# Performance work log

Measured on AMD Instinct MI355X. Metric: run time of the kernel, lower is better.

Reference implementation:

```python
import jax, jax.numpy as jnp
import numpy as np

B, F_IN, F_OUT, D, K = 32, 64, 64, 512, 64


def setup_inputs() -> dict:
    key = jax.random.key(0)
    k1, k2, k3 = jax.random.split(key, 3)
    x = jax.random.normal(k1, (B, F_IN, D), dtype=jnp.float32)
    # Evaluated monomial-word operators: K matrices of size D x D
    word_ops = jax.random.normal(k2, (K, D, D), dtype=jnp.float32)
    # nn.init.uniform_ -> U[0,1)
    coeff = jax.random.uniform(k3, (F_OUT, F_IN, K), dtype=jnp.float32)
    return {"x": x, "word_ops": word_ops, "coeff": coeff}


def reference(x, word_ops, coeff):
    # Per sample in the torch code:
    #   evals[i, d, k] = (X @ W_k)[i, d] = sum_e X[i, e] * W[k, e, d]
    #   res = tensordot(coeff, evals, ([1, 2], [0, 2]))  -> [F_out, D]
    # Fully batched fused contraction (replaces the Python loop over batch):
    # evals: [B, F_in, D, K]
    evals = jnp.einsum('bie,ked->bidk', x, word_ops)
    # out: [B, F_out, D]
    out = jnp.einsum('oik,bidk->bod', coeff, evals)
    return out
```

## Files before the change

kernel.cpp:

```cpp
#include <hip/hip_runtime.h>
#include <hip/hip_bf16.h>


#define KK 32768

typedef __attribute__((ext_vector_type(8))) short bf16x8;
typedef __attribute__((ext_vector_type(4))) float f32x4;

__device__ __forceinline__ unsigned short f2bf(float f) {
  unsigned int u = __float_as_uint(f);
  return (unsigned short)((u + 0x7FFFu + ((u >> 16) & 1u)) >> 16);
}

__device__ __forceinline__ unsigned int pkbf2(float a, float b) {
  __hip_bfloat162 h = __float22bfloat162_rn(make_float2(a, b));
  return *(unsigned int*)&h;
}

__device__ __forceinline__ void gld16(void* lds, const void* g) {
  __builtin_amdgcn_global_load_lds((const __attribute__((address_space(1))) void*)g,
                                   (__attribute__((address_space(3))) void*)lds,
                                   16, 0, 0);
}

#define WAIT_VM0_LG0() asm volatile("s_waitcnt vmcnt(0) lgkmcnt(0)" ::: "memory")
#define WAIT_VM4()     asm volatile("s_waitcnt vmcnt(4)" ::: "memory")
#define WAIT_LG0()     asm volatile("s_waitcnt lgkmcnt(0)" ::: "memory")
#define BARRIER()      __builtin_amdgcn_s_barrier()
#define SCHEDB()       __builtin_amdgcn_sched_barrier(0)

__global__ __launch_bounds__(256) void prep_kern(const float* __restrict__ x,
                                                 const float* __restrict__ c,
                                                 const float* __restrict__ W,
                                                 unsigned short* __restrict__ xT,
                                                 unsigned short* __restrict__ cb,
                                                 unsigned short* __restrict__ WbT) {
  __shared__ float tile[64][133];
  int bx = blockIdx.x;
  int t = threadIdx.x;
  if (bx < 2048) {
    int k = bx >> 5, et = (bx >> 2) & 7, dq = bx & 3;
    const float* src = W + ((size_t)k * 512 + (size_t)et * 64) * 512 + dq * 128;
    int rr = t >> 5, c4 = t & 31;
#pragma unroll
    for (int p = 0; p < 8; p++) {
      int e = p * 8 + rr;
      float4 v = *(const float4*)(src + (size_t)e * 512 + c4 * 4);
      *(float4*)&tile[e][c4 * 4] = v;
    }
    __syncthreads();
    int ch = t & 7, dr = t >> 3;
#pragma unroll
    for (int p = 0; p < 4; p++) {
      int d = p * 32 + dr, e0 = ch * 8;
      uint4 o4;
      o4.x = pkbf2(tile[e0 + 0][d], tile[e0 + 1][d]);
      o4.y = pkbf2(tile[e0 + 2][d], tile[e0 + 3][d]);
      o4.z = pkbf2(tile[e0 + 4][d], tile[e0 + 5][d]);
      o4.w = pkbf2(tile[e0 + 6][d], tile[e0 + 7][d]);
      *(uint4*)(WbT + (size_t)(dq * 128 + d) * KK + k * 512 + et * 64 + e0) = o4;
    }
  } else if (bx < 2176) {
    int bx2 = bx - 2048;
    int b = bx2 >> 2, ec = bx2 & 3;
    const float* src = x + (size_t)b * 32768 + ec * 128;
    int rr = t >> 5, c4 = t & 31;
#pragma unroll
    for (int p = 0; p < 8; p++) {
      int i = p * 8 + rr;
      float4 v = *(const float4*)(src + (size_t)i * 512 + c4 * 4);
      *(float4*)&tile[i][c4 * 4] = v;
    }
    __syncthreads();
    unsigned short* dst = xT + (size_t)b * 32768 + ec * 128 * 64;
    int ch = t & 7, er = t >> 3;
#pragma unroll
    for (int p = 0; p < 4; p++) {
      int e = p * 32 + er, i0 = ch * 8;
      uint4 o4;
      o4.x = pkbf2(tile[i0 + 0][e], tile[i0 + 1][e]);
      o4.y = pkbf2(tile[i0 + 2][e], tile[i0 + 3][e]);
      o4.z = pkbf2(tile[i0 + 4][e], tile[i0 + 5][e]);
      o4.w = pkbf2(tile[i0 + 6][e], tile[i0 + 7][e]);
      *(uint4*)(dst + e * 64 + i0) = o4;
    }
  } else {
    int rb = bx - 2176;
    unsigned short* lds = (unsigned short*)tile;
    const float* src = c + (size_t)rb * 4096;
#pragma unroll
    for (int j = 0; j < 16; j++) {
      int idx = j * 256 + t;
      int r = idx >> 6, k = idx & 63;
      lds[r * 66 + k] = f2bf(src[idx]);
    }
    __syncthreads();
#pragma unroll
    for (int j = 0; j < 16; j++) {
      int idx = j * 256 + t;
      int k = idx >> 6, r = idx & 63;
      cb[(size_t)k * 4096 + rb * 64 + r] = lds[r * 66 + k];
    }
  }
}

__global__ __launch_bounds__(256, 2) void fused_kern(const unsigned short* __restrict__ xT,
                                                     const unsigned short* __restrict__ cb,
                                                     const unsigned short* __restrict__ Bt,
                                                     float* __restrict__ out) {
  __shared__ unsigned short u[128 * 64];
  __shared__ unsigned short Bs0[128 * 64];
  __shared__ unsigned short Bs1[128 * 64];
  __shared__ unsigned short ck[4 * 64 * 64];
  int bx = blockIdx.x;
  int ks = bx & 15, np = (bx >> 4) & 1, mt = bx >> 5;
  int m0 = mt * 128, n0 = np * 256, kw0 = ks * 4, b0 = mt * 2;
  int t = threadIdx.x;
  int wid = t >> 6, lane = t & 63, q = lane >> 4, l16 = lane & 15;
  int wmb = wid & 1;
  int wnh = wid >> 1;
  int srow = t >> 3;
  int cg = (t & 7) ^ (srow & 7);
  {
    const unsigned short* gc = cb + (size_t)kw0 * 4096;
#pragma unroll
    for (int j = 0; j < 8; j++) {
      int row = j * 32 + srow;
      gld16((char*)ck + (j * 256 + t) * 16, gc + (size_t)row * 64 + cg * 8);
    }
    const unsigned short* gb = Bt + (size_t)n0 * KK + (size_t)kw0 * 512;
#pragma unroll
    for (int j = 0; j < 4; j++)
      gld16((char*)Bs0 + (j * 256 + t) * 16, gb + (size_t)(j * 32 + srow) * KK + cg * 8);
  }
  f32x4 acc[4][8] = {};
  bf16x8 ax[4][2];
#pragma unroll 1
  for (int s = 0; s < 32; s++) {
    int k = s & 3, ec = s >> 2;
    f32x4 td[4][2];
    const unsigned short* ckk = ck + k * 4096;
    if (k != 0) {
      bf16x8 bc[2][2];
#pragma unroll
      for (int otl = 0; otl < 2; otl++)
#pragma unroll
        for (int k2 = 0; k2 < 2; k2++) {
          int o = (wnh * 2 + otl) * 16 + l16;
          int s2 = (k2 * 4 + q) ^ (o & 7);
          bc[otl][k2] = *(const bf16x8*)(ckk + o * 64 + s2 * 8);
        }
#pragma unroll
      for (int et = 0; et < 4; et++)
#pragma unroll
        for (int otl = 0; otl < 2; otl++) {
          td[et][otl] = (f32x4){0.f, 0.f, 0.f, 0.f};
#pragma unroll
          for (int k2 = 0; k2 < 2; k2++)
            td[et][otl] = __builtin_amdgcn_mfma_f32_16x16x32_bf16(ax[et][k2], bc[otl][k2],
                                                                  td[et][otl], 0, 0, 0);
        }
      WAIT_VM0_LG0(); BARRIER(); SCHEDB();
      {
        const unsigned short* gb = Bt + (size_t)(n0 + 128) * KK
                                      + (size_t)(kw0 + k) * 512 + ec * 64;
#pragma unroll
        for (int j = 0; j < 4; j++)
          gld16((char*)Bs1 + (j * 256 + t) * 16, gb + (size_t)(j * 32 + srow) * KK + cg * 8);
      }
    } else {
      WAIT_VM0_LG0(); BARRIER(); SCHEDB();
#pragma unroll
      for (int j = 0; j < 4; j++) {
        int row = j * 32 + srow;
        int bl = row >> 6, el = row & 63;
        gld16((char*)u + (j * 256 + t) * 16,
              xT + (size_t)(b0 + bl) * 32768 + (size_t)(ec * 64 + el) * 64 + cg * 8);
      }
      {
        const unsigned short* gb = Bt + (size_t)(n0 + 128) * KK
                                      + (size_t)kw0 * 512 + ec * 64;
#pragma unroll
        for (int j = 0; j < 4; j++)
          gld16((char*)Bs1 + (j * 256 + t) * 16, gb + (size_t)(j * 32 + srow) * KK + cg * 8);
      }
      WAIT_VM4(); BARRIER(); SCHEDB();
#pragma unroll
      for (int et = 0; et < 4; et++)
#pragma unroll
        for (int k2 = 0; k2 < 2; k2++) {
          int row = wmb * 64 + et * 16 + l16;
          int s2 = (k2 * 4 + q) ^ (row & 7);
          ax[et][k2] = *(const bf16x8*)(u + row * 64 + s2 * 8);
        }
      bf16x8 bc[2][2];
#pragma unroll
      for (int otl = 0; otl < 2; otl++)
#pragma unroll
        for (int k2 = 0; k2 < 2; k2++) {
          int o = (wnh * 2 + otl) * 16 + l16;
          int s2 = (k2 * 4 + q) ^ (o & 7);
          bc[otl][k2] = *(const bf16x8*)(ckk + o * 64 + s2 * 8);
        }
#pragma unroll
      for (int et = 0; et < 4; et++)
#pragma unroll
        for (int otl = 0; otl < 2; otl++) {
          td[et][otl] = (f32x4){0.f, 0.f, 0.f, 0.f};
#pragma unroll
          for (int k2 = 0; k2 < 2; k2++)
            td[et][otl] = __builtin_amdgcn_mfma_f32_16x16x32_bf16(ax[et][k2], bc[otl][k2],
                                                                  td[et][otl], 0, 0, 0);
        }
      WAIT_LG0(); BARRIER(); SCHEDB();
    }
#pragma unroll
    for (int et = 0; et < 4; et++)
#pragma unroll
      for (int otl = 0; otl < 2; otl++) {
        int row = wmb * 64 + (wnh * 2 + otl) * 16 + l16;
        int c0 = et * 16 + q * 4;
        int phys = ((c0 >> 3) ^ (row & 7)) * 8 + (c0 & 7);
        uint2 v;
        v.x = pkbf2(td[et][otl][0], td[et][otl][1]);
        v.y = pkbf2(td[et][otl][2], td[et][otl][3]);
        *(uint2*)(u + row * 64 + phys) = v;
      }
    WAIT_LG0(); BARRIER(); SCHEDB();
#pragma unroll
    for (int k2 = 0; k2 < 2; k2++) {
      bf16x8 af[4], bfr[4];
#pragma unroll
      for (int mf = 0; mf < 4; mf++) {
        int row = wmb * 64 + mf * 16 + l16;
        af[mf] = *(const bf16x8*)(u + row * 64 + (((k2 * 4 + q) ^ (row & 7))) * 8);
      }
#pragma unroll
      for (int nf = 0; nf < 4; nf++) {
        int row = wnh * 64 + nf * 16 + l16;
        bfr[nf] = *(const bf16x8*)(Bs0 + row * 64 + (((k2 * 4 + q) ^ (row & 7))) * 8);
      }
      __builtin_amdgcn_s_setprio(1);
#pragma unroll
      for (int mf = 0; mf < 4; mf++)
#pragma unroll
        for (int nf = 0; nf < 4; nf++)
          acc[mf][nf] = __builtin_amdgcn_mfma_f32_16x16x32_bf16(af[mf], bfr[nf],
                                                                acc[mf][nf], 0, 0, 0);
      __builtin_amdgcn_s_setprio(0);
    }
    WAIT_VM0_LG0(); BARRIER(); SCHEDB();
    if (s < 31) {
      int sn = s + 1, kn = sn & 3, ecn = sn >> 2;
      const unsigned short* gb = Bt + (size_t)n0 * KK
                                    + (size_t)(kw0 + kn) * 512 + ecn * 64;
#pragma unroll
      for (int j = 0; j < 4; j++)
        gld16((char*)Bs0 + (j * 256 + t) * 16, gb + (size_t)(j * 32 + srow) * KK + cg * 8);
    }
#pragma unroll
    for (int k2 = 0; k2 < 2; k2++) {
      bf16x8 af[4], bfr[4];
#pragma unroll
      for (int mf = 0; mf < 4; mf++) {
        int row = wmb * 64 + mf * 16 + l16;
        af[mf] = *(const bf16x8*)(u + row * 64 + (((k2 * 4 + q) ^ (row & 7))) * 8);
      }
#pragma unroll
      for (int nf = 0; nf < 4; nf++) {
        int row = wnh * 64 + nf * 16 + l16;
        bfr[nf] = *(const bf16x8*)(Bs1 + row * 64 + (((k2 * 4 + q) ^ (row & 7))) * 8);
      }
      __builtin_amdgcn_s_setprio(1);
#pragma unroll
      for (int mf = 0; mf < 4; mf++)
#pragma unroll
        for (int nf = 0; nf < 4; nf++)
          acc[mf][4 + nf] = __builtin_amdgcn_mfma_f32_16x16x32_bf16(af[mf], bfr[nf],
                                                                    acc[mf][4 + nf], 0, 0, 0);
      __builtin_amdgcn_s_setprio(0);
    }
  }
#pragma unroll
  for (int mf = 0; mf < 4; mf++)
#pragma unroll
    for (int nf = 0; nf < 8; nf++) {
      int col = n0 + (nf >> 2) * 128 + wnh * 64 + (nf & 3) * 16 + l16;
#pragma unroll
      for (int r = 0; r < 4; r++)
        atomicAdd(&out[(size_t)(m0 + wmb * 64 + mf * 16 + q * 4 + r) * 512 + col],
                  acc[mf][nf][r]);
    }
}

__global__ __launch_bounds__(256) void fallback_kern(const float* __restrict__ x,
                                                     const float* __restrict__ W,
                                                     const float* __restrict__ coeff,
                                                     float* __restrict__ out) {
  __shared__ float ev[64][129];
  int b = blockIdx.x >> 6, k = blockIdx.x & 63;
  int t = threadIdx.x, dl = t & 127, half = t >> 7;
  const float* xb = x + (size_t)b * 64 * 512;
  const float* Wk = W + (size_t)k * 512 * 512;
  for (int dc = 0; dc < 4; dc++) {
    int d = dc * 128 + dl;
    for (int i = half * 32; i < half * 32 + 32; i++) {
      float acc = 0.f;
      const float* xr = xb + (size_t)i * 512;
#pragma unroll 4
      for (int e = 0; e < 512; e++) acc += xr[e] * Wk[(size_t)e * 512 + d];
      ev[i][dl] = acc;
    }
    __syncthreads();
    for (int o = half * 32; o < half * 32 + 32; o++) {
      float s = 0.f;
#pragma unroll 8
      for (int i = 0; i < 64; i++) s += coeff[((size_t)o * 64 + i) * 64 + k] * ev[i][dl];
      atomicAdd(&out[((size_t)(b * 64 + o)) * 512 + d], s);
    }
    __syncthreads();
  }
}

extern "C" void kernel_launch(void* const* d_in, const int* in_sizes, int n_in,
                              void* d_out, int out_size, void* d_ws, size_t ws_size,
                              hipStream_t stream) {
  const float* x = (const float*)d_in[0];
  const float* W = (const float*)d_in[1];
  const float* coeff = (const float*)d_in[2];
  float* out = (float*)d_out;
  const size_t OFF_XT = 33554432;
  const size_t OFF_CB = OFF_XT + 2097152;
  const size_t NEED = OFF_CB + 524288;

  hipMemsetAsync(d_out, 0, (size_t)out_size * sizeof(float), stream);
  if (ws_size >= NEED) {
    unsigned short* WbT = (unsigned short*)d_ws;
    unsigned short* xT  = (unsigned short*)((char*)d_ws + OFF_XT);
    unsigned short* cb  = (unsigned short*)((char*)d_ws + OFF_CB);
    prep_kern<<<2240, 256, 0, stream>>>(x, coeff, W, xT, cb, WbT);
    fused_kern<<<512, 256, 0, stream>>>(xT, cb, WbT, out);
  } else {
    fallback_kern<<<2048, 256, 0, stream>>>(x, W, coeff, out);
  }
}
```

Baseline: 218.4 us.

## Restructure fused GEMM pipeline: merged B tile loads, fewer barriers, staggered step order

Changes the fused kernel's schedule. Both 128-column B halves are now prefetched together at the end of each step, and each wave owns one whole half, issuing 32 MFMAs per k2 from a single LDS buffer. The x tile load moves into the prefetch phase, which removes a barrier pair and a separate wait per step. Blocks with an odd value of one grid-index bit start halfway through the 32-step sequence, likely so concurrent blocks read different parts of Bt and contend less on memory and atomics. The cost is more registers for the B fragments and a deeper outstanding load count.

```diff
diff --git a/kernel.cpp b/kernel.cpp
--- a/kernel.cpp
+++ b/kernel.cpp
@@ -24,7 +24,7 @@
 }
 
 #define WAIT_VM0_LG0() asm volatile("s_waitcnt vmcnt(0) lgkmcnt(0)" ::: "memory")
-#define WAIT_VM4()     asm volatile("s_waitcnt vmcnt(4)" ::: "memory")
+#define WAIT_VM8()     asm volatile("s_waitcnt vmcnt(8)" ::: "memory")
 #define WAIT_LG0()     asm volatile("s_waitcnt lgkmcnt(0)" ::: "memory")
 #define BARRIER()      __builtin_amdgcn_s_barrier()
 #define SCHEDB()       __builtin_amdgcn_sched_barrier(0)
@@ -109,8 +109,7 @@
                                                      const unsigned short* __restrict__ Bt,
                                                      float* __restrict__ out) {
   __shared__ unsigned short u[128 * 64];
-  __shared__ unsigned short Bs0[128 * 64];
-  __shared__ unsigned short Bs1[128 * 64];
+  __shared__ unsigned short Bs[2][128 * 64];
   __shared__ unsigned short ck[4 * 64 * 64];
   int bx = blockIdx.x;
   int ks = bx & 15, np = (bx >> 4) & 1, mt = bx >> 5;
@@ -121,6 +120,7 @@
   int wnh = wid >> 1;
   int srow = t >> 3;
   int cg = (t & 7) ^ (srow & 7);
+  int p = (bx >> 8) & 1, s0 = p * 16, ec0 = p * 4;
   {
     const unsigned short* gc = cb + (size_t)kw0 * 4096;
 #pragma unroll
@@ -128,19 +128,40 @@
       int row = j * 32 + srow;
       gld16((char*)ck + (j * 256 + t) * 16, gc + (size_t)row * 64 + cg * 8);
     }
-    const unsigned short* gb = Bt + (size_t)n0 * KK + (size_t)kw0 * 512;
+#pragma unroll
+    for (int j = 0; j < 4; j++) {
+      int row = j * 32 + srow;
+      int bl = row >> 6, el = row & 63;
+      gld16((char*)u + (j * 256 + t) * 16,
+            xT + (size_t)(b0 + bl) * 32768 + (size_t)(ec0 * 64 + el) * 64 + cg * 8);
+    }
+    const unsigned short* gb0 = Bt + (size_t)n0 * KK + (size_t)kw0 * 512 + ec0 * 64;
 #pragma unroll
     for (int j = 0; j < 4; j++)
-      gld16((char*)Bs0 + (j * 256 + t) * 16, gb + (size_t)(j * 32 + srow) * KK + cg * 8);
+      gld16((char*)Bs[0] + (j * 256 + t) * 16, gb0 + (size_t)(j * 32 + srow) * KK + cg * 8);
+    const unsigned short* gb1 = Bt + (size_t)(n0 + 128) * KK + (size_t)kw0 * 512 + ec0 * 64;
+#pragma unroll
+    for (int j = 0; j < 4; j++)
+      gld16((char*)Bs[1] + (j * 256 + t) * 16, gb1 + (size_t)(j * 32 + srow) * KK + cg * 8);
   }
   f32x4 acc[4][8] = {};
   bf16x8 ax[4][2];
 #pragma unroll 1
   for (int s = 0; s < 32; s++) {
-    int k = s & 3, ec = s >> 2;
+    int se = (s + s0) & 31;
+    int k = se & 3, ec = se >> 2;
+    const unsigned short* ckk = ck + k * 4096;
     f32x4 td[4][2];
-    const unsigned short* ckk = ck + k * 4096;
-    if (k != 0) {
+    if (k == 0) {
+      WAIT_VM8(); BARRIER(); SCHEDB();
+#pragma unroll
+      for (int et = 0; et < 4; et++)
+#pragma unroll
+        for (int k2 = 0; k2 < 2; k2++) {
+          int row = wmb * 64 + et * 16 + l16;
+          int s2 = (k2 * 4 + q) ^ (row & 7);
+          ax[et][k2] = *(const bf16x8*)(u + row * 64 + s2 * 8);
+        }
       bf16x8 bc[2][2];
 #pragma unroll
       for (int otl = 0; otl < 2; otl++)
@@ -150,6 +171,7 @@
           int s2 = (k2 * 4 + q) ^ (o & 7);
           bc[otl][k2] = *(const bf16x8*)(ckk + o * 64 + s2 * 8);
         }
+      __builtin_amdgcn_s_setprio(1);
 #pragma unroll
       for (int et = 0; et < 4; et++)
 #pragma unroll
@@ -160,39 +182,9 @@
             td[et][otl] = __builtin_amdgcn_mfma_f32_16x16x32_bf16(ax[et][k2], bc[otl][k2],
                                                                   td[et][otl], 0, 0, 0);
         }
-      WAIT_VM0_LG0(); BARRIER(); SCHEDB();
-      {
-        const unsigned short* gb = Bt + (size_t)(n0 + 128) * KK
-                                      + (size_t)(kw0 + k) * 512 + ec * 64;
-#pragma unroll
-        for (int j = 0; j < 4; j++)
-          gld16((char*)Bs1 + (j * 256 + t) * 16, gb + (size_t)(j * 32 + srow) * KK + cg * 8);
-      }
+      __builtin_amdgcn_s_setprio(0);
+      WAIT_LG0(); BARRIER(); SCHEDB();
     } else {
-      WAIT_VM0_LG0(); BARRIER(); SCHEDB();
-#pragma unroll
-      for (int j = 0; j < 4; j++) {
-        int row = j * 32 + srow;
-        int bl = row >> 6, el = row & 63;
-        gld16((char*)u + (j * 256 + t) * 16,
-              xT + (size_t)(b0 + bl) * 32768 + (size_t)(ec * 64 + el) * 64 + cg * 8);
-      }
-      {
-        const unsigned short* gb = Bt + (size_t)(n0 + 128) * KK
-                                      + (size_t)kw0 * 512 + ec * 64;
-#pragma unroll
-        for (int j = 0; j < 4; j++)
-          gld16((char*)Bs1 + (j * 256 + t) * 16, gb + (size_t)(j * 32 + srow) * KK + cg * 8);
-      }
-      WAIT_VM4(); BARRIER(); SCHEDB();
-#pragma unroll
-      for (int et = 0; et < 4; et++)
-#pragma unroll
-        for (int k2 = 0; k2 < 2; k2++) {
-          int row = wmb * 64 + et * 16 + l16;
-          int s2 = (k2 * 4 + q) ^ (row & 7);
-          ax[et][k2] = *(const bf16x8*)(u + row * 64 + s2 * 8);
-        }
       bf16x8 bc[2][2];
 #pragma unroll
       for (int otl = 0; otl < 2; otl++)
@@ -202,6 +194,7 @@
           int s2 = (k2 * 4 + q) ^ (o & 7);
           bc[otl][k2] = *(const bf16x8*)(ckk + o * 64 + s2 * 8);
         }
+      __builtin_amdgcn_s_setprio(1);
 #pragma unroll
       for (int et = 0; et < 4; et++)
 #pragma unroll
@@ -212,7 +205,7 @@
             td[et][otl] = __builtin_amdgcn_mfma_f32_16x16x32_bf16(ax[et][k2], bc[otl][k2],
                                                                   td[et][otl], 0, 0, 0);
         }
-      WAIT_LG0(); BARRIER(); SCHEDB();
+      __builtin_amdgcn_s_setprio(0);
     }
 #pragma unroll
     for (int et = 0; et < 4; et++)
@@ -226,71 +219,64 @@
         v.y = pkbf2(td[et][otl][2], td[et][otl][3]);
         *(uint2*)(u + row * 64 + phys) = v;
       }
+    WAIT_VM0_LG0(); BARRIER(); SCHEDB();
+    {
+      const unsigned short* bsw = Bs[wnh];
+#pragma unroll
+      for (int k2 = 0; k2 < 2; k2++) {
+        bf16x8 af[4], bfr[8];
+#pragma unroll
+        for (int mf = 0; mf < 4; mf++) {
+          int row = wmb * 64 + mf * 16 + l16;
+          af[mf] = *(const bf16x8*)(u + row * 64 + (((k2 * 4 + q) ^ (row & 7))) * 8);
+        }
+#pragma unroll
+        for (int nf = 0; nf < 8; nf++) {
+          int row = nf * 16 + l16;
+          bfr[nf] = *(const bf16x8*)(bsw + row * 64 + (((k2 * 4 + q) ^ (row & 7))) * 8);
+        }
+        __builtin_amdgcn_s_setprio(1);
+#pragma unroll
+        for (int mf = 0; mf < 4; mf++)
+#pragma unroll
+          for (int nf = 0; nf < 8; nf++)
+            acc[mf][nf] = __builtin_amdgcn_mfma_f32_16x16x32_bf16(af[mf], bfr[nf],
+                                                                  acc[mf][nf], 0, 0, 0);
+        __builtin_amdgcn_s_setprio(0);
+      }
+    }
     WAIT_LG0(); BARRIER(); SCHEDB();
-#pragma unroll
-    for (int k2 = 0; k2 < 2; k2++) {
-      bf16x8 af[4], bfr[4];
-#pragma unroll
-      for (int mf = 0; mf < 4; mf++) {
-        int row = wmb * 64 + mf * 16 + l16;
-        af[mf] = *(const bf16x8*)(u + row * 64 + (((k2 * 4 + q) ^ (row & 7))) * 8);
+    if (s < 31) {
+      int sn = (s + 1 + s0) & 31, kn = sn & 3, ecn = sn >> 2;
+      if (kn == 0) {
+#pragma unroll
+        for (int j = 0; j < 4; j++) {
+          int row = j * 32 + srow;
+          int bl = row >> 6, el = row & 63;
+          gld16((char*)u + (j * 256 + t) * 16,
+                xT + (size_t)(b0 + bl) * 32768 + (size_t)(ecn * 64 + el) * 64 + cg * 8);
+        }
       }
-#pragma unroll
-      for (int nf = 0; nf < 4; nf++) {
-        int row = wnh * 64 + nf * 16 + l16;
-        bfr[nf] = *(const bf16x8*)(Bs0 + row * 64 + (((k2 * 4 + q) ^ (row & 7))) * 8);
-      }
-      __builtin_amdgcn_s_setprio(1);
-#pragma unroll
-      for (int mf = 0; mf < 4; mf++)
-#pragma unroll
-        for (int nf = 0; nf < 4; nf++)
-          acc[mf][nf] = __builtin_amdgcn_mfma_f32_16x16x32_bf16(af[mf], bfr[nf],
-                                                                acc[mf][nf], 0, 0, 0);
-      __builtin_amdgcn_s_setprio(0);
-    }
-    WAIT_VM0_LG0(); BARRIER(); SCHEDB();
-    if (s < 31) {
-      int sn = s + 1, kn = sn & 3, ecn = sn >> 2;
-      const unsigned short* gb = Bt + (size_t)n0 * KK
-                                    + (size_t)(kw0 + kn) * 512 + ecn * 64;
+      const unsigned short* gb0 = Bt + (size_t)n0 * KK + (size_t)(kw0 + kn) * 512 + ecn * 64;
 #pragma unroll
       for (int j = 0; j < 4; j++)
-        gld16((char*)Bs0 + (j * 256 + t) * 16, gb + (size_t)(j * 32 + srow) * KK + cg * 8);
-    }
-#pragma unroll
-    for (int k2 = 0; k2 < 2; k2++) {
-      bf16x8 af[4], bfr[4];
-#pragma unroll
-      for (int mf = 0; mf < 4; mf++) {
-        int row = wmb * 64 + mf * 16 + l16;
-        af[mf] = *(const bf16x8*)(u + row * 64 + (((k2 * 4 + q) ^ (row & 7))) * 8);
-      }
-#pragma unroll
-      for (int nf = 0; nf < 4; nf++) {
-        int row = wnh * 64 + nf * 16 + l16;
-        bfr[nf] = *(const bf16x8*)(Bs1 + row * 64 + (((k2 * 4 + q) ^ (row & 7))) * 8);
-      }
-      __builtin_amdgcn_s_setprio(1);
-#pragma unroll
-      for (int mf = 0; mf < 4; mf++)
-#pragma unroll
-        for (int nf = 0; nf < 4; nf++)
-          acc[mf][4 + nf] = __builtin_amdgcn_mfma_f32_16x16x32_bf16(af[mf], bfr[nf],
-                                                                    acc[mf][4 + nf], 0, 0, 0);
-      __builtin_amdgcn_s_setprio(0);
+        gld16((char*)Bs[0] + (j * 256 + t) * 16, gb0 + (size_t)(j * 32 + srow) * KK + cg * 8);
+      const unsigned short* gb1 = Bt + (size_t)(n0 + 128) * KK
+                                     + (size_t)(kw0 + kn) * 512 + ecn * 64;
+#pragma unroll
+      for (int j = 0; j < 4; j++)
+        gld16((char*)Bs[1] + (j * 256 + t) * 16, gb1 + (size_t)(j * 32 + srow) * KK + cg * 8);
     }
   }
 #pragma unroll
   for (int mf = 0; mf < 4; mf++)
 #pragma unroll
-    for (int nf = 0; nf < 8; nf++) {
-      int col = n0 + (nf >> 2) * 128 + wnh * 64 + (nf & 3) * 16 + l16;
+    for (int nf = 0; nf < 8; nf++)
 #pragma unroll
       for (int r = 0; r < 4; r++)
-        atomicAdd(&out[(size_t)(m0 + wmb * 64 + mf * 16 + q * 4 + r) * 512 + col],
+        atomicAdd(&out[(size_t)(m0 + wmb * 64 + mf * 16 + q * 4 + r) * 512
+                       + n0 + wnh * 128 + nf * 16 + l16],
                   acc[mf][nf][r]);
-    }
 }
 
 __global__ __launch_bounds__(256) void fallback_kern(const float* __restrict__ x,
```

Result: no change. 219.5 us (+0.5%).
